# Kernel tuning notes

Measured on AMD Instinct MI355X. Metric: run time of the kernel, lower is better.

Reference implementation:

```python
import jax, jax.numpy as jnp
import numpy as np

N_NODES = 100000
N_EDGES = 1600000
D_IN, D_HID, D_OUT = 128, 128, 64


def _mean_agg(h_src_feat, src, dst, num_nodes):
    # gather source features along edges, scatter-sum into destinations,
    # divide by in-degree (clamped to 1, matching DGL zero-degree handling)
    summed = jax.ops.segment_sum(h_src_feat[src], dst, num_segments=num_nodes)
    deg = jax.ops.segment_sum(jnp.ones((src.shape[0],), h_src_feat.dtype), dst,
                              num_segments=num_nodes)
    return summed / jnp.maximum(deg, 1.0)[:, None]


def setup_inputs() -> dict:
    key = jax.random.key(0)
    ks = jax.random.split(key, 8)
    x = jax.random.normal(ks[0], (N_NODES, D_IN), dtype=jnp.float32)
    src = jax.random.randint(ks[1], (N_EDGES,), 0, N_NODES, dtype=jnp.int64)
    dst = jax.random.randint(ks[2], (N_EDGES,), 0, N_NODES, dtype=jnp.int64)
    s1 = 1.0 / np.sqrt(D_IN)
    s2 = 1.0 / np.sqrt(D_HID)
    W_self1 = jax.random.normal(ks[3], (D_IN, D_HID), dtype=jnp.float32) * s1
    W_neigh1 = jax.random.normal(ks[4], (D_IN, D_HID), dtype=jnp.float32) * s1
    b1 = jnp.zeros((D_HID,), dtype=jnp.float32)
    W_self2 = jax.random.normal(ks[5], (D_HID, D_OUT), dtype=jnp.float32) * s2
    W_neigh2 = jax.random.normal(ks[6], (D_HID, D_OUT), dtype=jnp.float32) * s2
    b2 = jnp.zeros((D_OUT,), dtype=jnp.float32)
    return {"x": x, "src": src, "dst": dst,
            "W_self1": W_self1, "W_neigh1": W_neigh1, "b1": b1,
            "W_self2": W_self2, "W_neigh2": W_neigh2, "b2": b2}


def reference(x, src, dst, W_self1, W_neigh1, b1, W_self2, W_neigh2, b2):
    n = x.shape[0]
    # layer 1: SAGEConv(mean) + ReLU (dropout is identity in eval mode)
    agg1 = _mean_agg(x, src, dst, n)
    h = x @ W_self1 + agg1 @ W_neigh1 + b1
    h = jax.nn.relu(h)
    # layer 2: SAGEConv(mean)
    agg2 = _mean_agg(h, src, dst, n)
    out = h @ W_self2 + agg2 @ W_neigh2 + b2
    return out
```

## Files before the change

### kernel.cpp

```cpp
#include <hip/hip_runtime.h>

#define N_NODES 100000
#define N_EDGES 1600000
#define D 128
#define D_OUT 64
#define MAXDEG 64

#define NBUCK 782
#define BSHIFT 7
#define BCAP  3072
#define NBLK_SPLIT 500
#define CHUNK 3200
#define NBLK_PACK 25
#define GEMM_BLOCKS 1563

typedef __attribute__((ext_vector_type(8))) short short8;
typedef __attribute__((ext_vector_type(4))) float floatx4;
typedef __attribute__((ext_vector_type(2))) float floatx2;

__device__ inline unsigned short f2bf(float f) {
    unsigned u = __builtin_bit_cast(unsigned, f);
    u = (u + 0x7fffu + ((u >> 16) & 1u)) >> 16;
    return (unsigned short)u;
}
__device__ inline float bf2f(unsigned u16) {
    return __builtin_bit_cast(float, u16 << 16);
}

template<bool KPERM>
__device__ inline void pack_ncat(const float* __restrict__ Wa, const float* __restrict__ Wb,
                                 int ncA, int ncB, unsigned short* __restrict__ out, int t) {
    int nnt = (ncA + ncB) >> 4;
    int lane = t & 63;
    int nt = (t >> 6) % nnt;
    int kt = t / (64 * nnt);
    int col = nt * 16 + (lane & 15);
    int k0 = kt * 32 + ((lane >> 4) << 3);
    const float* W = (col < ncA) ? Wa : Wb;
    int nc = (col < ncA) ? ncA : ncB;
    int c  = (col < ncA) ? col : col - ncA;
    unsigned short* dstp = out + (size_t)((kt * nnt + nt) * 64 + lane) * 8;
    #pragma unroll
    for (int j = 0; j < 8; ++j) {
        int k = k0 + j;
        int kr = KPERM ? (((k & 7) << 4) | (k >> 3)) : k;
        dstp[j] = f2bf(W[(size_t)kr * nc + c]);
    }
}

__global__ __launch_bounds__(256) void split_pack(
        const int* __restrict__ src, const int* __restrict__ dst,
        int* __restrict__ gcur, int* __restrict__ bucketbuf,
        const float* __restrict__ Ws1, const float* __restrict__ Wn1,
        const float* __restrict__ Ws2, const float* __restrict__ Wn2,
        unsigned short* __restrict__ Wp1, unsigned short* __restrict__ Wp2,
        unsigned char* __restrict__ y8, unsigned char* __restrict__ z8) {
    __shared__ int cnt[NBUCK];
    __shared__ int base_s[NBUCK];
    __shared__ int dstc[CHUNK];
    const int tid = threadIdx.x;
    const int b = blockIdx.x;
    if (b < NBLK_SPLIT) {
        const int e0 = b * CHUNK;
        for (int i = tid; i < NBUCK; i += 256) cnt[i] = 0;
        __syncthreads();
        for (int i = tid; i < CHUNK; i += 256) {
            int d = __builtin_nontemporal_load(dst + e0 + i);
            dstc[i] = d;
            atomicAdd(&cnt[d >> BSHIFT], 1);
        }
        __syncthreads();
        for (int i = tid; i < NBUCK; i += 256) {
            int c = cnt[i];
            base_s[i] = c ? atomicAdd(&gcur[i], c) : 0;
            cnt[i] = 0;
        }
        __syncthreads();
        for (int i = tid; i < CHUNK; i += 256) {
            int d = dstc[i];
            int s = __builtin_nontemporal_load(src + e0 + i);
            int bk = d >> BSHIFT;
            int p = base_s[bk] + atomicAdd(&cnt[bk], 1);
            if (p < BCAP)
                bucketbuf[bk * BCAP + p] = ((d & 127) << 17) | s;
        }
    } else {
        int sub = b - NBLK_SPLIT;
        if (sub < 16)      pack_ncat<false>(Ws1, Wn1, D, D, Wp1, sub * 256 + tid);
        else if (sub < 24) pack_ncat<true >(Ws2, Wn2, D_OUT, D_OUT, Wp2, (sub - 16) * 256 + tid);
        else {
            if (tid < 32)       ((unsigned*)(y8 + (size_t)N_NODES * 128))[tid] = 0;
            else if (tid < 48)  ((unsigned*)(z8 + (size_t)N_NODES * 64))[tid - 32] = 0;
        }
    }
}

template<int NTA, int NTB, bool AF32, int ILV>
__device__ inline void gemm_body(int bid,
        const void* __restrict__ A, const unsigned short* __restrict__ Wp,
        const float* __restrict__ bias, void* __restrict__ OutA,
        unsigned char* __restrict__ OutB, int tid)
{
    const int NT = NTA + NTB;
    const int wave = tid >> 6;
    const int lane = tid & 63;
    const int q = lane >> 4, m = lane & 15;

    int row = bid * 64 + wave * 16 + m;
    int rowc = (row < N_NODES) ? row : (N_NODES - 1);

    floatx4 acc[NT];
    #pragma unroll
    for (int nt = 0; nt < NT; ++nt) acc[nt] = (floatx4){0.f, 0.f, 0.f, 0.f};

    #pragma unroll
    for (int kt = 0; kt < 4; ++kt) {
        short8 af;
        if (AF32) {
            const float* xr = (const float*)A + (size_t)rowc * D + kt * 32 + q * 8;
            float4 f0 = *(const float4*)xr;
            float4 f1 = *(const float4*)(xr + 4);
            af[0] = (short)f2bf(f0.x); af[1] = (short)f2bf(f0.y);
            af[2] = (short)f2bf(f0.z); af[3] = (short)f2bf(f0.w);
            af[4] = (short)f2bf(f1.x); af[5] = (short)f2bf(f1.y);
            af[6] = (short)f2bf(f1.z); af[7] = (short)f2bf(f1.w);
        } else {
            af = *(const short8*)((const unsigned short*)A +
                                  (size_t)rowc * D + kt * 32 + q * 8);
        }
        #pragma unroll
        for (int nt = 0; nt < NT; ++nt) {
            short8 bf = *(const short8*)(Wp + (size_t)((kt * NT + nt) * 64 + lane) * 8);
            acc[nt] = __builtin_amdgcn_mfma_f32_16x16x32_bf16(af, bf, acc[nt], 0, 0, 0);
        }
    }

    const int orow_base = bid * 64 + wave * 16 + q * 4;
    if (ILV == 1) {
        float bv[8];
        #pragma unroll
        for (int nt = 0; nt < 8; ++nt) bv[nt] = bias[nt * 16 + m];
        #pragma unroll
        for (int i = 0; i < 4; ++i) {
            int orow = orow_base + i;
            if (orow < N_NODES) {
                unsigned w[4];
                #pragma unroll
                for (int t = 0; t < 4; ++t) {
                    float v0 = acc[2 * t][i]     + bv[2 * t];
                    float v1 = acc[2 * t + 1][i] + bv[2 * t + 1];
                    w[t] = (unsigned)f2bf(v0) | ((unsigned)f2bf(v1) << 16);
                }
                uint4 pv; pv.x = w[0]; pv.y = w[1]; pv.z = w[2]; pv.w = w[3];
                *(uint4*)((unsigned short*)OutA + (size_t)orow * 128 + m * 8) = pv;
                int pk0 = __builtin_amdgcn_cvt_pk_fp8_f32(acc[8][i],  acc[9][i],  0,   false);
                pk0     = __builtin_amdgcn_cvt_pk_fp8_f32(acc[10][i], acc[11][i], pk0, true);
                int pk1 = __builtin_amdgcn_cvt_pk_fp8_f32(acc[12][i], acc[13][i], 0,   false);
                pk1     = __builtin_amdgcn_cvt_pk_fp8_f32(acc[14][i], acc[15][i], pk1, true);
                uint2 v8; v8.x = (unsigned)pk0; v8.y = (unsigned)pk1;
                *(uint2*)(OutB + (size_t)orow * 128 + m * 8) = v8;
            }
        }
    } else {
        float bv[4];
        #pragma unroll
        for (int nt = 0; nt < 4; ++nt) bv[nt] = bias[nt * 16 + m];
        #pragma unroll
        for (int i = 0; i < 4; ++i) {
            int orow = orow_base + i;
            if (orow < N_NODES) {
                float4 o;
                o.x = acc[0][i] + bv[0]; o.y = acc[1][i] + bv[1];
                o.z = acc[2][i] + bv[2]; o.w = acc[3][i] + bv[3];
                *(float4*)((float*)OutA + (size_t)orow * 64 + m * 4) = o;
                int pk = __builtin_amdgcn_cvt_pk_fp8_f32(acc[4][i], acc[5][i], 0,  false);
                pk     = __builtin_amdgcn_cvt_pk_fp8_f32(acc[6][i], acc[7][i], pk, true);
                *(unsigned*)(OutB + (size_t)orow * 64 + m * 4) = (unsigned)pk;
            }
        }
    }
}

__global__ __launch_bounds__(256) void gemm1_csr(
        const float* __restrict__ x, const unsigned short* __restrict__ Wp1,
        const float* __restrict__ b1, unsigned short* __restrict__ xs,
        unsigned char* __restrict__ y8,
        const int* __restrict__ gcur, const int* __restrict__ bucketbuf,
        int* __restrict__ dcount, int* __restrict__ csrp)
{
    __shared__ int lcnt[128];
    const int tid = threadIdx.x;
    if (blockIdx.x < GEMM_BLOCKS) {
        gemm_body<8, 8, true, 1>(blockIdx.x, x, Wp1, b1, xs, y8, tid);
    } else {
        const int b = blockIdx.x - GEMM_BLOCKS;
        if (tid < 128) lcnt[tid] = 0;
        __syncthreads();
        int m = gcur[b]; if (m > BCAP) m = BCAP;
        const int* __restrict__ buf = bucketbuf + b * BCAP;
        for (int i = tid; i < m; i += 256) {
            int v = buf[i];
            int dloc = (v >> 17) & 127, s = v & 0x1FFFF;
            int node = (b << BSHIFT) + dloc;
            int slot = atomicAdd(&lcnt[dloc], 1);
            if (slot < MAXDEG && node < N_NODES)
                csrp[((size_t)node << 6) + slot] = s;
        }
        __syncthreads();
        if (tid < 128) {
            int node = (b << BSHIFT) + tid;
            if (node < N_NODES) {
                int c = lcnt[tid]; if (c > MAXDEG) c = MAXDEG;
                dcount[node] = c;
                int cf = (c + 15) & ~15; if (cf > MAXDEG) cf = MAXDEG;
                int* row = csrp + ((size_t)node << 6);
                for (int k = c; k < cf; ++k) row[k] = N_NODES;
            }
        }
    }
}

__global__ __launch_bounds__(256) void gemm2(
        const unsigned short* __restrict__ h, const unsigned short* __restrict__ Wp2,
        const float* __restrict__ b2, float* __restrict__ tmp,
        unsigned char* __restrict__ z8)
{
    gemm_body<4, 4, false, 2>(blockIdx.x, h, Wp2, b2, tmp, z8, threadIdx.x);
}

template<bool L1>
__global__ __launch_bounds__(256) void agg_add(
        const unsigned char* __restrict__ feat, const int* __restrict__ csrp,
        const int* __restrict__ dcount, const void* __restrict__ self,
        void* __restrict__ out)
{
    const int LPE = L1 ? 32 : 16;
    const int EPG = 64 / LPE;
    const int FSH = L1 ? 7 : 6;
    const int NC  = L1 ? 128 : 64;

    int w = (blockIdx.x * 256 + threadIdx.x) >> 6;
    int lane = threadIdx.x & 63;
    if (w >= N_NODES) return;
    int dg = __builtin_amdgcn_readfirstlane(dcount[w]);
    int cf = (dg + 15) & ~15;
    const int g = lane / LPE;
    const int l = lane % LPE;
    int idxv = 0;
    if (lane < cf) idxv = csrp[((size_t)w << 6) + lane];

    floatx2 ac0 = (floatx2){0.f, 0.f};
    floatx2 ac1 = (floatx2){0.f, 0.f};
    for (int j = 0; j < dg; j += 16) {
        #pragma unroll
        for (int u = 0; u < 16 / EPG; ++u) {
            int s = __shfl(idxv, j + u * EPG + g);
            unsigned v = *(const unsigned*)(feat + ((size_t)s << FSH) + (l << 2));
            ac0 += __builtin_amdgcn_cvt_pk_f32_fp8(v, false);
            ac1 += __builtin_amdgcn_cvt_pk_f32_fp8(v, true);
        }
    }
    #pragma unroll
    for (int delta = 32; delta >= LPE; delta >>= 1) {
        ac0.x += __shfl_down(ac0.x, delta); ac0.y += __shfl_down(ac0.y, delta);
        ac1.x += __shfl_down(ac1.x, delta); ac1.y += __shfl_down(ac1.y, delta);
    }
    if (g == 0) {
        float invd = (dg > 0) ? 1.0f / (float)dg : 1.0f;
        if (L1) {
            uint2 sv = *(const uint2*)((const unsigned short*)self + (size_t)w * NC + l * 4);
            float h0 = bf2f(sv.x & 0xffffu)  + ac0.x * invd;
            float h1 = bf2f(sv.x >> 16)      + ac0.y * invd;
            float h2 = bf2f(sv.y & 0xffffu)  + ac1.x * invd;
            float h3 = bf2f(sv.y >> 16)      + ac1.y * invd;
            h0 = fmaxf(h0, 0.f); h1 = fmaxf(h1, 0.f);
            h2 = fmaxf(h2, 0.f); h3 = fmaxf(h3, 0.f);
            uint2 pv;
            pv.x = (unsigned)f2bf(h0) | ((unsigned)f2bf(h1) << 16);
            pv.y = (unsigned)f2bf(h2) | ((unsigned)f2bf(h3) << 16);
            *(uint2*)((unsigned short*)out + (size_t)w * NC + l * 4) = pv;
        } else {
            const float* sp = (const float*)self + (size_t)w * NC + l * 4;
            float4 s0 = *(const float4*)sp;
            float v0 = s0.x + ac0.x * invd;
            float v1 = s0.y + ac0.y * invd;
            float v2 = s0.z + ac1.x * invd;
            float v3 = s0.w + ac1.y * invd;
            float* op = (float*)out + (size_t)w * NC;
            op[l]      = v0;
            op[16 + l] = v1;
            op[32 + l] = v2;
            op[48 + l] = v3;
        }
    }
}

extern "C" void kernel_launch(void* const* d_in, const int* in_sizes, int n_in,
                              void* d_out, int out_size, void* d_ws, size_t ws_size,
                              hipStream_t stream) {
    const float* x   = (const float*)d_in[0];
    const int*   src = (const int*)d_in[1];
    const int*   dst = (const int*)d_in[2];
    const float* Ws1 = (const float*)d_in[3];
    const float* Wn1 = (const float*)d_in[4];
    const float* b1  = (const float*)d_in[5];
    const float* Ws2 = (const float*)d_in[6];
    const float* Wn2 = (const float*)d_in[7];
    const float* b2  = (const float*)d_in[8];
    float* out = (float*)d_out;

    const size_t nd = (size_t)N_NODES * D;
    unsigned short* h   = (unsigned short*)d_ws;
    unsigned short* xs  = h + nd;
    float*          tmp = (float*)xs;
    unsigned char*  y8  = (unsigned char*)(xs + nd);
    unsigned char*  z8  = y8 + (size_t)(N_NODES + 1) * D;
    int* dcount = (int*)(z8 + (size_t)(N_NODES + 1) * D_OUT);
    int* csrp   = dcount + N_NODES;
    int* gcur   = csrp + (size_t)N_NODES * MAXDEG;
    int* bucketbuf = gcur + 1024;
    unsigned short* Wp1 = (unsigned short*)(bucketbuf + (size_t)NBUCK * BCAP);
    unsigned short* Wp2 = Wp1 + 32768;

    hipMemsetAsync(gcur, 0, NBUCK * sizeof(int), stream);

    split_pack<<<NBLK_SPLIT + NBLK_PACK, 256, 0, stream>>>(
        src, dst, gcur, bucketbuf, Ws1, Wn1, Ws2, Wn2, Wp1, Wp2, y8, z8);

    const int agg_blocks = (N_NODES * 64 + 255) / 256;

    gemm1_csr<<<GEMM_BLOCKS + NBUCK, 256, 0, stream>>>(
        x, Wp1, b1, xs, y8, gcur, bucketbuf, dcount, csrp);
    agg_add<true ><<<agg_blocks, 256, 0, stream>>>(y8, csrp, dcount, xs, h);
    gemm2<<<GEMM_BLOCKS, 256, 0, stream>>>(h, Wp2, b2, tmp, z8);
    agg_add<false><<<agg_blocks, 256, 0, stream>>>(z8, csrp, dcount, tmp, out);
}
```

Measured before the change: 274.7 us.

## Use hardware bf16 pack conversion, reorder fused blocks, and double split blocks

Replaces the software round-to-nearest-even bf16 conversion with the v_cvt_pk_bf16_f32 instruction in the GEMM A-load, GEMM1 epilogue and layer-1 aggregation output. It puts the CSR-build blocks ahead of the GEMM blocks in the fused launch so the irregular scatter work is dispatched first. It also doubles the number of edge-split blocks and halves their chunk size to spread the bucketing over more blocks. The hardware conversion needs an architecture that supports the instruction, and its rounding may differ slightly from the software path.

Measured after the change: 284.5 us. 3.6% more time.

```diff
diff --git a/kernel.cpp b/kernel.cpp
--- a/kernel.cpp
+++ b/kernel.cpp
@@ -9,14 +9,15 @@
 #define NBUCK 782
 #define BSHIFT 7
 #define BCAP  3072
-#define NBLK_SPLIT 500
-#define CHUNK 3200
+#define NBLK_SPLIT 1000
+#define CHUNK 1600
 #define NBLK_PACK 25
 #define GEMM_BLOCKS 1563
 
 typedef __attribute__((ext_vector_type(8))) short short8;
 typedef __attribute__((ext_vector_type(4))) float floatx4;
 typedef __attribute__((ext_vector_type(2))) float floatx2;
+typedef __attribute__((ext_vector_type(4))) unsigned uint32x4;
 
 __device__ inline unsigned short f2bf(float f) {
     unsigned u = __builtin_bit_cast(unsigned, f);
@@ -25,6 +26,11 @@
 }
 __device__ inline float bf2f(unsigned u16) {
     return __builtin_bit_cast(float, u16 << 16);
+}
+__device__ inline unsigned cvt_pk_bf16(float lo, float hi) {
+    unsigned r;
+    asm("v_cvt_pk_bf16_f32 %0, %1, %2" : "=v"(r) : "v"(lo), "v"(hi));
+    return r;
 }
 
 template<bool KPERM>
@@ -120,10 +126,12 @@
             const float* xr = (const float*)A + (size_t)rowc * D + kt * 32 + q * 8;
             float4 f0 = *(const float4*)xr;
             float4 f1 = *(const float4*)(xr + 4);
-            af[0] = (short)f2bf(f0.x); af[1] = (short)f2bf(f0.y);
-            af[2] = (short)f2bf(f0.z); af[3] = (short)f2bf(f0.w);
-            af[4] = (short)f2bf(f1.x); af[5] = (short)f2bf(f1.y);
-            af[6] = (short)f2bf(f1.z); af[7] = (short)f2bf(f1.w);
+            uint32x4 t;
+            t[0] = cvt_pk_bf16(f0.x, f0.y);
+            t[1] = cvt_pk_bf16(f0.z, f0.w);
+            t[2] = cvt_pk_bf16(f1.x, f1.y);
+            t[3] = cvt_pk_bf16(f1.z, f1.w);
+            af = __builtin_bit_cast(short8, t);
         } else {
             af = *(const short8*)((const unsigned short*)A +
                                   (size_t)rowc * D + kt * 32 + q * 8);
@@ -144,15 +152,12 @@
         for (int i = 0; i < 4; ++i) {
             int orow = orow_base + i;
             if (orow < N_NODES) {
-                unsigned w[4];
+                uint32x4 pv;
                 #pragma unroll
-                for (int t = 0; t < 4; ++t) {
-                    float v0 = acc[2 * t][i]     + bv[2 * t];
-                    float v1 = acc[2 * t + 1][i] + bv[2 * t + 1];
-                    w[t] = (unsigned)f2bf(v0) | ((unsigned)f2bf(v1) << 16);
-                }
-                uint4 pv; pv.x = w[0]; pv.y = w[1]; pv.z = w[2]; pv.w = w[3];
-                *(uint4*)((unsigned short*)OutA + (size_t)orow * 128 + m * 8) = pv;
+                for (int t = 0; t < 4; ++t)
+                    pv[t] = cvt_pk_bf16(acc[2 * t][i]     + bv[2 * t],
+                                        acc[2 * t + 1][i] + bv[2 * t + 1]);
+                *(uint32x4*)((unsigned short*)OutA + (size_t)orow * 128 + m * 8) = pv;
                 int pk0 = __builtin_amdgcn_cvt_pk_fp8_f32(acc[8][i],  acc[9][i],  0,   false);
                 pk0     = __builtin_amdgcn_cvt_pk_fp8_f32(acc[10][i], acc[11][i], pk0, true);
                 int pk1 = __builtin_amdgcn_cvt_pk_fp8_f32(acc[12][i], acc[13][i], 0,   false);
@@ -190,10 +195,8 @@
 {
     __shared__ int lcnt[128];
     const int tid = threadIdx.x;
-    if (blockIdx.x < GEMM_BLOCKS) {
-        gemm_body<8, 8, true, 1>(blockIdx.x, x, Wp1, b1, xs, y8, tid);
-    } else {
-        const int b = blockIdx.x - GEMM_BLOCKS;
+    if (blockIdx.x < NBUCK) {
+        const int b = blockIdx.x;
         if (tid < 128) lcnt[tid] = 0;
         __syncthreads();
         int m = gcur[b]; if (m > BCAP) m = BCAP;
@@ -217,6 +220,8 @@
                 for (int k = c; k < cf; ++k) row[k] = N_NODES;
             }
         }
+    } else {
+        gemm_body<8, 8, true, 1>(blockIdx.x - NBUCK, x, Wp1, b1, xs, y8, tid);
     }
 }
 
@@ -276,8 +281,8 @@
             h0 = fmaxf(h0, 0.f); h1 = fmaxf(h1, 0.f);
             h2 = fmaxf(h2, 0.f); h3 = fmaxf(h3, 0.f);
             uint2 pv;
-            pv.x = (unsigned)f2bf(h0) | ((unsigned)f2bf(h1) << 16);
-            pv.y = (unsigned)f2bf(h2) | ((unsigned)f2bf(h3) << 16);
+            pv.x = cvt_pk_bf16(h0, h1);
+            pv.y = cvt_pk_bf16(h2, h3);
             *(uint2*)((unsigned short*)out + (size_t)w * NC + l * 4) = pv;
         } else {
             const float* sp = (const float*)self + (size_t)w * NC + l * 4;
@@ -329,7 +334,7 @@
 
     const int agg_blocks = (N_NODES * 64 + 255) / 256;
 
-    gemm1_csr<<<GEMM_BLOCKS + NBUCK, 256, 0, stream>>>(
+    gemm1_csr<<<NBUCK + GEMM_BLOCKS, 256, 0, stream>>>(
         x, Wp1, b1, xs, y8, gcur, bucketbuf, dcount, csrp);
     agg_add<true ><<<agg_blocks, 256, 0, stream>>>(y8, csrp, dcount, xs, h);
     gemm2<<<GEMM_BLOCKS, 256, 0, stream>>>(h, Wp2, b2, tmp, z8);
```
